# Optimization experiments

Measured on AMD Instinct MI355X. Metric: run time of the kernel, lower is better.

Reference implementation:

```python
import jax, jax.numpy as jnp
import numpy as np

CAT_VOCAB = 1000
TYPE_VOCAB = 10
EMB = 64
PROJ = 16
MAX_SUB = 8
SENT = 3
W1_OUT = 32
H_IN = PROJ + SENT + PROJ + 1 + 1  # 37


def setup_inputs() -> dict:
    key = jax.random.key(0)
    ks = jax.random.split(key, 24)
    Nt, Nh = 65536, 262144
    inp = {
        "cat_t": jax.random.randint(ks[0], (Nt,), 0, CAT_VOCAB, dtype=jnp.int32),
        "sub_t": jax.random.randint(ks[1], (Nt, MAX_SUB), 0, CAT_VOCAB, dtype=jnp.int32),
        "sub_len_t": jax.random.randint(ks[2], (Nt,), 1, MAX_SUB + 1, dtype=jnp.int32),
        "sentiment_t": jax.random.uniform(ks[3], (Nt, SENT), dtype=jnp.float32),
        "type_t": jax.random.randint(ks[4], (Nt,), 0, TYPE_VOCAB, dtype=jnp.int32),
        "cat_h": jax.random.randint(ks[5], (Nh,), 0, CAT_VOCAB, dtype=jnp.int32),
        "sub_h": jax.random.randint(ks[6], (Nh, MAX_SUB), 0, CAT_VOCAB, dtype=jnp.int32),
        "sub_len_h": jax.random.randint(ks[7], (Nh,), 1, MAX_SUB + 1, dtype=jnp.int32),
        "sentiment_h": jax.random.uniform(ks[8], (Nh, SENT), dtype=jnp.float32),
        "type_h": jax.random.randint(ks[9], (Nh,), 0, TYPE_VOCAB, dtype=jnp.int32),
        "read_time_h": jax.random.uniform(ks[10], (Nh, 1), dtype=jnp.float32),
        "scroll_h": jax.random.uniform(ks[11], (Nh, 1), dtype=jnp.float32),
        # learned params
        "cat_emb": jax.random.normal(ks[12], (CAT_VOCAB, EMB), dtype=jnp.float32) * 0.02,
        "cat_W": jax.random.normal(ks[13], (EMB, PROJ), dtype=jnp.float32) / np.sqrt(EMB),
        "cat_b": jnp.zeros((PROJ,), dtype=jnp.float32),
        "type_emb": jax.random.normal(ks[14], (TYPE_VOCAB, EMB), dtype=jnp.float32) * 0.02,
        "type_W": jax.random.normal(ks[15], (EMB, PROJ), dtype=jnp.float32) / np.sqrt(EMB),
        "type_b": jnp.zeros((PROJ,), dtype=jnp.float32),
        "w1_W": jax.random.normal(ks[16], (H_IN, W1_OUT), dtype=jnp.float32) / np.sqrt(H_IN),
        "w1_b": jnp.zeros((W1_OUT,), dtype=jnp.float32),
    }
    return inp


def _cat_feature(cat_idx, sub_idx, sub_len, emb, W, b):
    # category_embedding(cat) + mean_i category_embedding(sub_i)  (ragged mean via mask)
    base = emb[cat_idx] @ W + b                             # [N, 16]
    g = emb[sub_idx]                                        # [N, S, 64] (dominant gather)
    mask = (jnp.arange(MAX_SUB)[None, :] < sub_len[:, None]).astype(g.dtype)  # [N, S]
    denom = jnp.maximum(sub_len, 1).astype(g.dtype)[:, None]
    sub_mean = jnp.einsum('nse,ns->ne', g, mask) / denom    # [N, 64]
    return base + (sub_mean @ W + b)                        # mean of affine == affine of mean


def reference(cat_t, sub_t, sub_len_t, sentiment_t, type_t,
              cat_h, sub_h, sub_len_h, sentiment_h, type_h,
              read_time_h, scroll_h,
              cat_emb, cat_W, cat_b, type_emb, type_W, type_b, w1_W, w1_b):
    # target branch
    ct = _cat_feature(cat_t, sub_t, sub_len_t, cat_emb, cat_W, cat_b)
    tt = type_emb[type_t] @ type_W + type_b
    x_t = jnp.concatenate((ct, sentiment_t, tt), axis=1)    # [Nt, 35]
    # history branch
    ch = _cat_feature(cat_h, sub_h, sub_len_h, cat_emb, cat_W, cat_b)
    th = type_emb[type_h] @ type_W + type_b
    x_h = jnp.concatenate((ch, sentiment_h, th, read_time_h, scroll_h), axis=1) @ w1_W + w1_b
    return x_t, x_h
```

## Files before the change

### kernel.cpp

```cpp
#include <hip/hip_runtime.h>


#define OFF_PCAT  0
#define OFF_PTYPE 16000
#define OFF_QCAT  16384
#define OFF_QTYPE 48384
#define OFF_C0    48704

#define TBLK_T 256
#define TBLK_H 1792

__device__ __forceinline__ float4 f4add(float4 a, float4 b) {
    return make_float4(a.x + b.x, a.y + b.y, a.z + b.z, a.w + b.w);
}
__device__ __forceinline__ float4 f4fma(float s, float4 a, float4 c) {
    return make_float4(fmaf(s, a.x, c.x), fmaf(s, a.y, c.y),
                       fmaf(s, a.z, c.z), fmaf(s, a.w, c.w));
}

__global__ __launch_bounds__(256) void precompute_tables(
    const float* __restrict__ cat_emb, const float* __restrict__ cat_W,
    const float* __restrict__ cat_b,   const float* __restrict__ type_emb,
    const float* __restrict__ type_W,  const float* __restrict__ type_b,
    const float* __restrict__ w1_W,    const float* __restrict__ w1_b,
    float* __restrict__ ws)
{
    __shared__ float sWc[64 * 16];
    __shared__ float sWt[64 * 16];
    __shared__ float sW1[37 * 32];
    __shared__ float sEmb[16][65];
    __shared__ float sP[16][17];

    const int tid = threadIdx.x;
    for (int i = tid; i < 64 * 16; i += 256) { sWc[i] = cat_W[i]; sWt[i] = type_W[i]; }
    for (int i = tid; i < 37 * 32; i += 256) sW1[i] = w1_W[i];

    const int r   = tid >> 4;
    const int k   = tid & 15;
    const int row = blockIdx.x * 16 + r;
    const bool is_cat = (row < 1000);
    const bool valid  = (row < 1010);

    if (valid) {
        const float* src = is_cat ? (cat_emb + (size_t)row * 64)
                                  : (type_emb + (size_t)(row - 1000) * 64);
        const float4 v = ((const float4*)src)[k];
        sEmb[r][k * 4 + 0] = v.x; sEmb[r][k * 4 + 1] = v.y;
        sEmb[r][k * 4 + 2] = v.z; sEmb[r][k * 4 + 3] = v.w;
    }
    __syncthreads();

    float p = 0.f;
    if (valid) {
        const float* sW = is_cat ? sWc : sWt;
#pragma unroll 8
        for (int e = 0; e < 64; ++e)
            p = fmaf(sEmb[r][e], sW[e * 16 + k], p);
        if (is_cat) ws[OFF_PCAT + row * 16 + k] = p;
        else        ws[OFF_PTYPE + (row - 1000) * 16 + k] = p;
    }
    sP[r][k] = p;
    __syncthreads();

    if (valid) {
        const int woff = is_cat ? 0 : 19;
        float q0 = 0.f, q1 = 0.f;
#pragma unroll
        for (int kk = 0; kk < 16; ++kk) {
            const float pv = sP[r][kk];
            q0 = fmaf(pv, sW1[(woff + kk) * 32 + k], q0);
            q1 = fmaf(pv, sW1[(woff + kk) * 32 + k + 16], q1);
        }
        if (is_cat) {
            ws[OFF_QCAT + row * 32 + k]      = q0;
            ws[OFF_QCAT + row * 32 + k + 16] = q1;
        } else {
            ws[OFF_QTYPE + (row - 1000) * 32 + k]      = q0;
            ws[OFF_QTYPE + (row - 1000) * 32 + k + 16] = q1;
        }
    }

    if (blockIdx.x == 0 && tid < 32) {
        float c = w1_b[tid];
#pragma unroll
        for (int kk = 0; kk < 16; ++kk) c = fmaf(2.f * cat_b[kk], sW1[kk * 32 + tid], c);
#pragma unroll
        for (int kk = 0; kk < 16; ++kk) c = fmaf(type_b[kk], sW1[(19 + kk) * 32 + tid], c);
        ws[OFF_C0 + tid] = c;
    }
}

__global__ __launch_bounds__(256, 8) void news_main(
    const int* __restrict__ cat_t, const int* __restrict__ sub_t,
    const int* __restrict__ sub_len_t, const float* __restrict__ sent_t,
    const int* __restrict__ type_t,
    const int* __restrict__ cat_h, const int* __restrict__ sub_h,
    const int* __restrict__ sub_len_h, const float* __restrict__ sent_h,
    const int* __restrict__ type_h,
    const float* __restrict__ rt_h, const float* __restrict__ sc_h,
    const float* __restrict__ cat_b, const float* __restrict__ type_b,
    const float* __restrict__ w1_W,
    const float* __restrict__ ws, float* __restrict__ out,
    int Nt, int Nh, int nTilesT, int nTilesH)
{
    __shared__ float stage[64 * 36];
    __shared__ float wl[6 * 32];

    const float4* P4  = (const float4*)(ws + OFF_PCAT);
    const float4* PT4 = (const float4*)(ws + OFF_PTYPE);
    const float4* Q4  = (const float4*)(ws + OFF_QCAT);
    const float4* QT4 = (const float4*)(ws + OFF_QTYPE);
    const float*  c0  = ws + OFF_C0;

    const int tid = threadIdx.x;
    const int b   = blockIdx.x;

    if (b < TBLK_T) {
        const int g  = tid >> 2;
        const int sl = tid & 3;
        for (int tile = b; tile < nTilesT; tile += TBLK_T) {
            const int n = tile * 64 + g;
            if (n < Nt) {
                const int cat = cat_t[n];
                const int ty  = type_t[n];
                int len = sub_len_t[n];
                if (len < 1) len = 1;
                const int4* sp = (const int4*)(sub_t + (size_t)n * 8);
                const int4 sa = sp[0];
                const int4 sb = sp[1];

                float4 a = P4[cat * 4 + sl];
                float4 s = make_float4(0, 0, 0, 0);
                s = f4add(s, P4[sa.x * 4 + sl]);
                if (len > 1) s = f4add(s, P4[sa.y * 4 + sl]);
                if (len > 2) s = f4add(s, P4[sa.z * 4 + sl]);
                if (len > 3) s = f4add(s, P4[sa.w * 4 + sl]);
                if (len > 4) s = f4add(s, P4[sb.x * 4 + sl]);
                if (len > 5) s = f4add(s, P4[sb.y * 4 + sl]);
                if (len > 6) s = f4add(s, P4[sb.z * 4 + sl]);
                if (len > 7) s = f4add(s, P4[sb.w * 4 + sl]);

                const float inv = 1.0f / (float)len;
                a = f4fma(inv, s, a);
                a = f4fma(2.f, ((const float4*)cat_b)[sl], a);
                float4 t = f4add(PT4[ty * 4 + sl], ((const float4*)type_b)[sl]);

                float* row = stage + g * 36;
                ((float4*)row)[sl] = a;
                row[19 + sl * 4 + 0] = t.x;
                row[19 + sl * 4 + 1] = t.y;
                row[19 + sl * 4 + 2] = t.z;
                row[19 + sl * 4 + 3] = t.w;
                if (sl == 0) {
                    row[16] = sent_t[(size_t)n * 3 + 0];
                    row[17] = sent_t[(size_t)n * 3 + 1];
                    row[18] = sent_t[(size_t)n * 3 + 2];
                }
            }
            __syncthreads();
            int rows = Nt - tile * 64;
            if (rows > 64) rows = 64;
            const int cnt = rows * 35;
            const size_t base = (size_t)tile * 64 * 35;
            for (int i = tid; i < cnt; i += 256) {
                const int r2 = i / 35;
                const int c2 = i - r2 * 35;
                out[base + i] = stage[r2 * 36 + c2];
            }
            __syncthreads();
        }
    } else {
        if (tid < 192) {
            const int rr = tid >> 5, cc = tid & 31;
            const int srow = (rr < 3) ? (16 + rr) : (35 + (rr - 3));
            wl[tid] = (rr < 5) ? w1_W[srow * 32 + cc] : c0[cc];
        }
        __syncthreads();
        const int g  = tid >> 3;
        const int sl = tid & 7;
        float4* ob = (float4*)(out + (size_t)Nt * 35);
        const float4* wl4 = (const float4*)wl;

        for (int tile = b - TBLK_T; tile < nTilesH; tile += TBLK_H) {
            const int n = tile * 32 + g;
            if (n < Nh) {
                const int cat = cat_h[n];
                const int ty  = type_h[n];
                int len = sub_len_h[n];
                if (len < 1) len = 1;
                const int4* sp = (const int4*)(sub_h + (size_t)n * 8);
                const int4 sa = sp[0];
                const int4 sb = sp[1];

                float4 q = Q4[cat * 8 + sl];
                float4 s = make_float4(0, 0, 0, 0);
                s = f4add(s, Q4[sa.x * 8 + sl]);
                if (len > 1) s = f4add(s, Q4[sa.y * 8 + sl]);
                if (len > 2) s = f4add(s, Q4[sa.z * 8 + sl]);
                if (len > 3) s = f4add(s, Q4[sa.w * 8 + sl]);
                if (len > 4) s = f4add(s, Q4[sb.x * 8 + sl]);
                if (len > 5) s = f4add(s, Q4[sb.y * 8 + sl]);
                if (len > 6) s = f4add(s, Q4[sb.z * 8 + sl]);
                if (len > 7) s = f4add(s, Q4[sb.w * 8 + sl]);

                const float inv = 1.0f / (float)len;
                q = f4fma(inv, s, q);
                q = f4add(q, QT4[ty * 8 + sl]);

                const float se0 = sent_h[(size_t)n * 3 + 0];
                const float se1 = sent_h[(size_t)n * 3 + 1];
                const float se2 = sent_h[(size_t)n * 3 + 2];
                const float rtv = rt_h[n];
                const float scv = sc_h[n];
                q = f4fma(se0, wl4[0 * 8 + sl], q);
                q = f4fma(se1, wl4[1 * 8 + sl], q);
                q = f4fma(se2, wl4[2 * 8 + sl], q);
                q = f4fma(rtv, wl4[3 * 8 + sl], q);
                q = f4fma(scv, wl4[4 * 8 + sl], q);
                q = f4add(q,   wl4[5 * 8 + sl]);

                ob[(size_t)n * 8 + sl] = q;
            }
        }
    }
}

extern "C" void kernel_launch(void* const* d_in, const int* in_sizes, int n_in,
                              void* d_out, int out_size, void* d_ws, size_t ws_size,
                              hipStream_t stream) {
    const int*   cat_t     = (const int*)d_in[0];
    const int*   sub_t     = (const int*)d_in[1];
    const int*   sub_len_t = (const int*)d_in[2];
    const float* sent_t    = (const float*)d_in[3];
    const int*   type_t    = (const int*)d_in[4];
    const int*   cat_h     = (const int*)d_in[5];
    const int*   sub_h     = (const int*)d_in[6];
    const int*   sub_len_h = (const int*)d_in[7];
    const float* sent_h    = (const float*)d_in[8];
    const int*   type_h    = (const int*)d_in[9];
    const float* rt_h      = (const float*)d_in[10];
    const float* sc_h      = (const float*)d_in[11];
    const float* cat_emb   = (const float*)d_in[12];
    const float* cat_W     = (const float*)d_in[13];
    const float* cat_b     = (const float*)d_in[14];
    const float* type_emb  = (const float*)d_in[15];
    const float* type_W    = (const float*)d_in[16];
    const float* type_b    = (const float*)d_in[17];
    const float* w1_W      = (const float*)d_in[18];
    const float* w1_b      = (const float*)d_in[19];

    float* ws  = (float*)d_ws;
    float* out = (float*)d_out;
    const int Nt = in_sizes[0];
    const int Nh = in_sizes[5];

    precompute_tables<<<64, 256, 0, stream>>>(cat_emb, cat_W, cat_b,
                                              type_emb, type_W, type_b,
                                              w1_W, w1_b, ws);

    const int nTilesT = (Nt + 63) / 64;
    const int nTilesH = (Nh + 31) / 32;
    news_main<<<TBLK_T + TBLK_H, 256, 0, stream>>>(
        cat_t, sub_t, sub_len_t, sent_t, type_t,
        cat_h, sub_h, sub_len_h, sent_h, type_h,
        rt_h, sc_h, cat_b, type_b, w1_W,
        ws, out, Nt, Nh, nTilesT, nTilesH);
}
```

Baseline: 33.23 us.

## Stage projected lookup tables in LDS with padded rows, use 1024-thread blocks

Each block now copies the precomputed projected category and type tables (Q for history, P for target) into shared memory, with rows padded to avoid bank conflicts. The gathers then read LDS instead of global/L2. Blocks grow to 1024 threads over far fewer blocks (200 history, 56 target), and tiles grow accordingly. Each block pays a one-time table load of about 143 KB (history) or 80 KB (target). The large shared footprint limits occupancy to one block per CU, which may hurt latency hiding.

```diff
diff --git a/kernel.cpp b/kernel.cpp
--- a/kernel.cpp
+++ b/kernel.cpp
@@ -7,8 +7,9 @@
 #define OFF_QTYPE 48384
 #define OFF_C0    48704
 
-#define TBLK_T 256
-#define TBLK_H 1792
+#define HBLK 200
+#define TBLK 56
+#define SMEM_FLOATS 36552
 
 __device__ __forceinline__ float4 f4add(float4 a, float4 b) {
     return make_float4(a.x + b.x, a.y + b.y, a.z + b.z, a.w + b.w);
@@ -90,7 +91,7 @@
     }
 }
 
-__global__ __launch_bounds__(256, 8) void news_main(
+__global__ __launch_bounds__(1024, 4) void news_main(
     const int* __restrict__ cat_t, const int* __restrict__ sub_t,
     const int* __restrict__ sub_len_t, const float* __restrict__ sent_t,
     const int* __restrict__ type_t,
@@ -103,23 +104,101 @@
     const float* __restrict__ ws, float* __restrict__ out,
     int Nt, int Nh, int nTilesT, int nTilesH)
 {
-    __shared__ float stage[64 * 36];
-    __shared__ float wl[6 * 32];
-
-    const float4* P4  = (const float4*)(ws + OFF_PCAT);
-    const float4* PT4 = (const float4*)(ws + OFF_PTYPE);
-    const float4* Q4  = (const float4*)(ws + OFF_QCAT);
-    const float4* QT4 = (const float4*)(ws + OFF_QTYPE);
-    const float*  c0  = ws + OFF_C0;
+    __shared__ float smem[SMEM_FLOATS];
 
     const int tid = threadIdx.x;
     const int b   = blockIdx.x;
 
-    if (b < TBLK_T) {
+    if (b < HBLK) {
+        float4* lq4  = (float4*)smem;
+        float4* lqt4 = (float4*)(smem + 36000);
+        float*  wl   = smem + 36360;
+
+        const float4* Qs  = (const float4*)(ws + OFF_QCAT);
+        const float4* QTs = (const float4*)(ws + OFF_QTYPE);
+        for (int i = tid; i < 8000; i += 1024) {
+            const int r = i >> 3, j = i & 7;
+            lq4[r * 9 + j] = Qs[i];
+        }
+        if (tid < 80) {
+            const int r = tid >> 3, j = tid & 7;
+            lqt4[r * 9 + j] = QTs[tid];
+        }
+        if (tid < 192) {
+            const int rr = tid >> 5, cc = tid & 31;
+            const int srow = (rr < 3) ? (16 + rr) : (35 + (rr - 3));
+            wl[tid] = (rr < 5) ? w1_W[srow * 32 + cc] : ws[OFF_C0 + cc];
+        }
+        __syncthreads();
+
+        const int g  = tid >> 3;
+        const int sl = tid & 7;
+        float4* ob = (float4*)(out + (size_t)Nt * 35);
+        const float4* wl4 = (const float4*)wl;
+
+        for (int tile = b; tile < nTilesH; tile += HBLK) {
+            const int n = tile * 128 + g;
+            if (n < Nh) {
+                const int cat = cat_h[n];
+                const int ty  = type_h[n];
+                int len = sub_len_h[n];
+                if (len < 1) len = 1;
+                const int4* sp = (const int4*)(sub_h + (size_t)n * 8);
+                const int4 sa = sp[0];
+                const int4 sb = sp[1];
+
+                float4 q = lq4[cat * 9 + sl];
+                float4 s = make_float4(0, 0, 0, 0);
+                s = f4add(s, lq4[sa.x * 9 + sl]);
+                if (len > 1) s = f4add(s, lq4[sa.y * 9 + sl]);
+                if (len > 2) s = f4add(s, lq4[sa.z * 9 + sl]);
+                if (len > 3) s = f4add(s, lq4[sa.w * 9 + sl]);
+                if (len > 4) s = f4add(s, lq4[sb.x * 9 + sl]);
+                if (len > 5) s = f4add(s, lq4[sb.y * 9 + sl]);
+                if (len > 6) s = f4add(s, lq4[sb.z * 9 + sl]);
+                if (len > 7) s = f4add(s, lq4[sb.w * 9 + sl]);
+
+                const float inv = 1.0f / (float)len;
+                q = f4fma(inv, s, q);
+                q = f4add(q, lqt4[ty * 9 + sl]);
+
+                const float se0 = sent_h[(size_t)n * 3 + 0];
+                const float se1 = sent_h[(size_t)n * 3 + 1];
+                const float se2 = sent_h[(size_t)n * 3 + 2];
+                const float rtv = rt_h[n];
+                const float scv = sc_h[n];
+                q = f4fma(se0, wl4[0 * 8 + sl], q);
+                q = f4fma(se1, wl4[1 * 8 + sl], q);
+                q = f4fma(se2, wl4[2 * 8 + sl], q);
+                q = f4fma(rtv, wl4[3 * 8 + sl], q);
+                q = f4fma(scv, wl4[4 * 8 + sl], q);
+                q = f4add(q,   wl4[5 * 8 + sl]);
+
+                ob[(size_t)n * 8 + sl] = q;
+            }
+        }
+    } else {
+        float4* lp4   = (float4*)smem;
+        float4* lpt4  = (float4*)(smem + 20000);
+        float*  stage = smem + 20200;
+
+        const float4* Ps  = (const float4*)(ws + OFF_PCAT);
+        const float4* PTs = (const float4*)(ws + OFF_PTYPE);
+        for (int i = tid; i < 4000; i += 1024) {
+            const int r = i >> 2, j = i & 3;
+            lp4[r * 5 + j] = Ps[i];
+        }
+        if (tid < 40) {
+            const int r = tid >> 2, j = tid & 3;
+            lpt4[r * 5 + j] = PTs[tid];
+        }
+        __syncthreads();
+
         const int g  = tid >> 2;
         const int sl = tid & 3;
-        for (int tile = b; tile < nTilesT; tile += TBLK_T) {
-            const int n = tile * 64 + g;
+
+        for (int tile = b - HBLK; tile < nTilesT; tile += TBLK) {
+            const int n = tile * 256 + g;
             if (n < Nt) {
                 const int cat = cat_t[n];
                 const int ty  = type_t[n];
@@ -129,21 +208,21 @@
                 const int4 sa = sp[0];
                 const int4 sb = sp[1];
 
-                float4 a = P4[cat * 4 + sl];
+                float4 a = lp4[cat * 5 + sl];
                 float4 s = make_float4(0, 0, 0, 0);
-                s = f4add(s, P4[sa.x * 4 + sl]);
-                if (len > 1) s = f4add(s, P4[sa.y * 4 + sl]);
-                if (len > 2) s = f4add(s, P4[sa.z * 4 + sl]);
-                if (len > 3) s = f4add(s, P4[sa.w * 4 + sl]);
-                if (len > 4) s = f4add(s, P4[sb.x * 4 + sl]);
-                if (len > 5) s = f4add(s, P4[sb.y * 4 + sl]);
-                if (len > 6) s = f4add(s, P4[sb.z * 4 + sl]);
-                if (len > 7) s = f4add(s, P4[sb.w * 4 + sl]);
+                s = f4add(s, lp4[sa.x * 5 + sl]);
+                if (len > 1) s = f4add(s, lp4[sa.y * 5 + sl]);
+                if (len > 2) s = f4add(s, lp4[sa.z * 5 + sl]);
+                if (len > 3) s = f4add(s, lp4[sa.w * 5 + sl]);
+                if (len > 4) s = f4add(s, lp4[sb.x * 5 + sl]);
+                if (len > 5) s = f4add(s, lp4[sb.y * 5 + sl]);
+                if (len > 6) s = f4add(s, lp4[sb.z * 5 + sl]);
+                if (len > 7) s = f4add(s, lp4[sb.w * 5 + sl]);
 
                 const float inv = 1.0f / (float)len;
                 a = f4fma(inv, s, a);
                 a = f4fma(2.f, ((const float4*)cat_b)[sl], a);
-                float4 t = f4add(PT4[ty * 4 + sl], ((const float4*)type_b)[sl]);
+                float4 t = f4add(lpt4[ty * 5 + sl], ((const float4*)type_b)[sl]);
 
                 float* row = stage + g * 36;
                 ((float4*)row)[sl] = a;
@@ -158,69 +237,16 @@
                 }
             }
             __syncthreads();
-            int rows = Nt - tile * 64;
-            if (rows > 64) rows = 64;
+            int rows = Nt - tile * 256;
+            if (rows > 256) rows = 256;
             const int cnt = rows * 35;
-            const size_t base = (size_t)tile * 64 * 35;
-            for (int i = tid; i < cnt; i += 256) {
+            const size_t base = (size_t)tile * 256 * 35;
+            for (int i = tid; i < cnt; i += 1024) {
                 const int r2 = i / 35;
                 const int c2 = i - r2 * 35;
                 out[base + i] = stage[r2 * 36 + c2];
             }
             __syncthreads();
-        }
-    } else {
-        if (tid < 192) {
-            const int rr = tid >> 5, cc = tid & 31;
-            const int srow = (rr < 3) ? (16 + rr) : (35 + (rr - 3));
-            wl[tid] = (rr < 5) ? w1_W[srow * 32 + cc] : c0[cc];
-        }
-        __syncthreads();
-        const int g  = tid >> 3;
-        const int sl = tid & 7;
-        float4* ob = (float4*)(out + (size_t)Nt * 35);
-        const float4* wl4 = (const float4*)wl;
-
-        for (int tile = b - TBLK_T; tile < nTilesH; tile += TBLK_H) {
-            const int n = tile * 32 + g;
-            if (n < Nh) {
-                const int cat = cat_h[n];
-                const int ty  = type_h[n];
-                int len = sub_len_h[n];
-                if (len < 1) len = 1;
-                const int4* sp = (const int4*)(sub_h + (size_t)n * 8);
-                const int4 sa = sp[0];
-                const int4 sb = sp[1];
-
-                float4 q = Q4[cat * 8 + sl];
-                float4 s = make_float4(0, 0, 0, 0);
-                s = f4add(s, Q4[sa.x * 8 + sl]);
-                if (len > 1) s = f4add(s, Q4[sa.y * 8 + sl]);
-                if (len > 2) s = f4add(s, Q4[sa.z * 8 + sl]);
-                if (len > 3) s = f4add(s, Q4[sa.w * 8 + sl]);
-                if (len > 4) s = f4add(s, Q4[sb.x * 8 + sl]);
-                if (len > 5) s = f4add(s, Q4[sb.y * 8 + sl]);
-                if (len > 6) s = f4add(s, Q4[sb.z * 8 + sl]);
-                if (len > 7) s = f4add(s, Q4[sb.w * 8 + sl]);
-
-                const float inv = 1.0f / (float)len;
-                q = f4fma(inv, s, q);
-                q = f4add(q, QT4[ty * 8 + sl]);
-
-                const float se0 = sent_h[(size_t)n * 3 + 0];
-                const float se1 = sent_h[(size_t)n * 3 + 1];
-                const float se2 = sent_h[(size_t)n * 3 + 2];
-                const float rtv = rt_h[n];
-                const float scv = sc_h[n];
-                q = f4fma(se0, wl4[0 * 8 + sl], q);
-                q = f4fma(se1, wl4[1 * 8 + sl], q);
-                q = f4fma(se2, wl4[2 * 8 + sl], q);
-                q = f4fma(rtv, wl4[3 * 8 + sl], q);
-                q = f4fma(scv, wl4[4 * 8 + sl], q);
-                q = f4add(q,   wl4[5 * 8 + sl]);
-
-                ob[(size_t)n * 8 + sl] = q;
-            }
         }
     }
 }
@@ -258,9 +284,9 @@
                                               type_emb, type_W, type_b,
                                               w1_W, w1_b, ws);
 
-    const int nTilesT = (Nt + 63) / 64;
-    const int nTilesH = (Nh + 31) / 32;
-    news_main<<<TBLK_T + TBLK_H, 256, 0, stream>>>(
+    const int nTilesT = (Nt + 255) / 256;
+    const int nTilesH = (Nh + 127) / 128;
+    news_main<<<HBLK + TBLK, 1024, 0, stream>>>(
         cat_t, sub_t, sub_len_t, sent_t, type_t,
         cat_h, sub_h, sub_len_h, sent_h, type_h,
         rt_h, sc_h, cat_b, type_b, w1_W,
```

New measurement: 31.10 us. 6.4% less time.
